# Optimization experiments

Hardware: AMD Instinct MI355X
Metric: run time of the kernel (lower is better)

## Reference

```python
import jax, jax.numpy as jnp
import numpy as np

B, N_T, D_A, D_V, D_U = 64, 8192, 2, 64, 1
L, MODES, X_PAD = 4, 64, 8


def setup_inputs() -> dict:
    key = jax.random.key(0)
    ks = jax.random.split(key, 9)
    scale = 1.0 / (D_V * D_V)  # Xavier-style gain used in original
    return {
        "v": jax.random.normal(ks[0], (B, N_T), dtype=jnp.float32),
        "grid": jax.random.uniform(ks[1], (N_T,), dtype=jnp.float32),
        "p_w": jax.random.normal(ks[2], (D_A, D_V), dtype=jnp.float32) * 0.1,
        "p_b": jnp.zeros((D_V,), dtype=jnp.float32),
        "fw": jax.random.normal(ks[3], (L, D_V, D_V, MODES, 2), dtype=jnp.float32) * scale,
        "w_w": jax.random.normal(ks[4], (L, D_V, D_V), dtype=jnp.float32) * (1.0 / np.sqrt(D_V)),
        "w_b": jnp.zeros((L, D_V), dtype=jnp.float32),
        "q_w": jax.random.normal(ks[5], (D_V, D_U), dtype=jnp.float32) * (1.0 / np.sqrt(D_V)),
        "q_b": jnp.zeros((D_U,), dtype=jnp.float32),
    }


def _fourier_layer(x, w):
    # x: (B, C, n), w: (C, C, modes, 2) real/imag channel-mixing weights
    n = x.shape[-1]
    xf = jnp.fft.rfft(x)                      # (B, C, n//2+1) complex
    xm = xf[:, :, :MODES]
    xr, xi = jnp.real(xm), jnp.imag(xm)
    wr, wi = w[..., 0], w[..., 1]
    out_r = jnp.einsum('bix,iox->box', xr, wr) - jnp.einsum('bix,iox->box', xi, wi)
    out_i = jnp.einsum('bix,iox->box', xi, wr) + jnp.einsum('bix,iox->box', xr, wi)
    out_m = jax.lax.complex(out_r, out_i)     # (B, C, modes)
    out_ft = jnp.pad(out_m, ((0, 0), (0, 0), (0, n // 2 + 1 - MODES)))
    return jnp.fft.irfft(out_ft, n=n)         # (B, C, n)


def reference(v, grid, p_w, p_b, fw, w_w, w_b, q_w, q_b):
    b, n = v.shape
    # lift: concat signal with coordinate channel -> (B, n, 2)
    x = jnp.concatenate([v[:, :, None], jnp.broadcast_to(grid[None, :, None], (b, n, 1))], axis=-1)
    x = x @ p_w + p_b                          # (B, n, d_v)
    x = jnp.transpose(x, (0, 2, 1))            # (B, d_v, n)
    x = jnp.pad(x, ((0, 0), (0, 0), (0, X_PAD)))
    for i in range(L):
        x1 = _fourier_layer(x, fw[i])
        x2 = jnp.einsum('bcn,cd->bdn', x, w_w[i]) + w_b[i][None, :, None]
        x = x1 + x2
        if i < L - 1:
            x = jax.nn.relu(x)
    x = x[..., :-X_PAD]                        # remove padding
    out = jnp.einsum('bcn,cd->bnd', x, q_w) + q_b  # (B, n, d_u)
    return out[..., 0]                         # d_u == 1 -> squeeze
```

## Files before the change

### kernel.cpp

```cpp
#include <hip/hip_runtime.h>

#define NT    8192
#define NP    8200
#define NPP   8320
#define NB    64
#define DV    64
#define NL    4
#define TFR   520
#define KSP   20
#define SPB   13
#define PI2   6.28318530717958647692f

typedef _Float16 half8 __attribute__((ext_vector_type(8)));
typedef _Float16 half4 __attribute__((ext_vector_type(4)));
typedef float    f32x4 __attribute__((ext_vector_type(4)));

static const size_t B_XT   = 0;
static const size_t B_TABF = 68157440ull;
static const size_t B_TABI = B_TABF + 2129920ull;
static const size_t B_WFR  = B_TABI + 2129920ull;
static const size_t B_ZFR  = B_WFR  + 131072ull;
static const size_t B_XPF  = B_ZFR  + 1048576ull;
static const size_t B_VP   = B_XPF  + 20971520ull;
static const size_t B_G    = B_VP   + 327680ull;
static const size_t B_A    = B_G    + 512ull;

__global__ void k_prep(_Float16* __restrict__ tabF, _Float16* __restrict__ tabI) {
    int idx = blockIdx.x * 256 + threadIdx.x;
    if (idx >= NPP * 64) return;
    int t = idx >> 6, k = idx & 63;
    float c = 0.f, s = 0.f;
    if (t < NP) {
        int m = (int)(((long long)t * (long long)k) % NP);
        float th = (float)m * (PI2 / (float)NP);
        sincosf(th, &s, &c);
    }
    float al = (k == 0) ? (1.f / NP) : (2.f / NP);
    {
        int gs = t >> 5, lh = (t >> 3) & 3, j = t & 7;
        int m0 = 2 * k, m1 = 2 * k + 1;
        tabF[(((size_t)gs * 8 + (m0 >> 4)) * 64 + (m0 & 15) + 16 * lh) * 8 + j] = (_Float16)c;
        tabF[(((size_t)gs * 8 + (m1 >> 4)) * 64 + (m1 & 15) + 16 * lh) * 8 + j] = (_Float16)s;
    }
    {
        int tf = t >> 4, lt = t & 15;
        int m0 = 2 * k, m1 = 2 * k + 1;
        tabI[(((size_t)(m0 >> 5) * TFR + tf) * 64 + lt + 16 * ((m0 >> 3) & 3)) * 8 + (m0 & 7)] = (_Float16)(al * c);
        tabI[(((size_t)(m1 >> 5) * TFR + tf) * 64 + lt + 16 * ((m1 >> 3) & 3)) * 8 + (m1 & 7)] = (_Float16)(al * s);
    }
}

__global__ void k_prep_w(const float* __restrict__ ww, _Float16* __restrict__ Wfrag) {
    int idx = blockIdx.x * 256 + threadIdx.x;
    if (idx >= NL * DV * DV) return;
    int l = idx >> 12, cd = idx & 4095, c = cd >> 6, d = cd & 63;
    float wv = ww[((size_t)l * DV + c) * DV + d];
    _Float16 h = (_Float16)wv;
    _Float16 lo = (_Float16)(wv - (float)h);
    int ks = c >> 5, mf = d >> 4;
    int lane = (d & 15) + 16 * ((c >> 3) & 3), j = c & 7;
    Wfrag[((((size_t)l * 2 + 0) * 2 + ks) * 4 + mf) * 512 + (size_t)lane * 8 + j] = h;
    Wfrag[((((size_t)l * 2 + 1) * 2 + ks) * 4 + mf) * 512 + (size_t)lane * 8 + j] = lo;
}

__global__ void k_prep_p(const float* __restrict__ pw, const float* __restrict__ pb,
                         const float* __restrict__ ww, float* __restrict__ A) {
    int d = threadIdx.x;
    float a0 = 0.f, a1 = 0.f, a2 = 0.f;
    #pragma unroll 8
    for (int c = 0; c < DV; ++c) {
        float w = ww[(size_t)c * DV + d];
        a0 = fmaf(pw[c], w, a0);
        a1 = fmaf(pw[DV + c], w, a1);
        a2 = fmaf(pb[c], w, a2);
    }
    A[d] = a0; A[64 + d] = a1; A[128 + d] = a2;
}

__global__ void k_gd(const float* __restrict__ grd, float* __restrict__ G) {
    __shared__ float rb[256];
    int m = blockIdx.x, k = m >> 1, comp = m & 1;
    int tid = threadIdx.x;
    float s = 0.f;
    for (int t = tid; t < NT; t += 256) {
        int mm = (int)(((long long)t * (long long)k) % NP);
        float th = (float)mm * (PI2 / (float)NP);
        float sn, cs; sincosf(th, &sn, &cs);
        s += grd[t] * (comp ? sn : cs);
    }
    rb[tid] = s; __syncthreads();
    for (int h = 128; h > 0; h >>= 1) { if (tid < h) rb[tid] += rb[tid + h]; __syncthreads(); }
    if (tid == 0) G[m] = rb[0];
}

__launch_bounds__(256)
__global__ void k_fdft_v(const float* __restrict__ v, const _Float16* __restrict__ tabF,
                         _Float16* __restrict__ Vp) {
    int ksb = blockIdx.x;
    int tid = threadIdx.x, w = tid >> 6, lane = tid & 63, g = lane >> 4, r = lane & 15;
    const half8* tFv = (const half8*)tabF;
    f32x4 acc[4][2];
    #pragma unroll
    for (int mf = 0; mf < 4; ++mf)
        #pragma unroll
        for (int nf = 0; nf < 2; ++nf) acc[mf][nf] = (f32x4){0.f, 0.f, 0.f, 0.f};
    for (int s = 0; s < SPB; ++s) {
        int gs = ksb * SPB + s;
        int t0 = gs * 32 + g * 8;
        half8 a[4];
        #pragma unroll
        for (int mf = 0; mf < 4; ++mf) {
            int brow = mf * 16 + r;
            half8 hv;
            if (t0 < NT) {
                const float4* pv = (const float4*)&v[(size_t)brow * NT + t0];
                float4 v0 = pv[0], v1 = pv[1];
                hv[0] = (_Float16)v0.x; hv[1] = (_Float16)v0.y; hv[2] = (_Float16)v0.z; hv[3] = (_Float16)v0.w;
                hv[4] = (_Float16)v1.x; hv[5] = (_Float16)v1.y; hv[6] = (_Float16)v1.z; hv[7] = (_Float16)v1.w;
            } else {
                #pragma unroll
                for (int j = 0; j < 8; ++j) hv[j] = (_Float16)0.f;
            }
            a[mf] = hv;
        }
        half8 bb[2];
        #pragma unroll
        for (int nf = 0; nf < 2; ++nf) bb[nf] = tFv[((size_t)gs * 8 + w * 2 + nf) * 64 + lane];
        #pragma unroll
        for (int mf = 0; mf < 4; ++mf)
            #pragma unroll
            for (int nf = 0; nf < 2; ++nf)
                acc[mf][nf] = __builtin_amdgcn_mfma_f32_16x16x32_f16(a[mf], bb[nf], acc[mf][nf], 0, 0, 0);
    }
    #pragma unroll
    for (int mf = 0; mf < 4; ++mf)
        #pragma unroll
        for (int nf = 0; nf < 2; ++nf)
            #pragma unroll
            for (int reg = 0; reg < 4; ++reg) {
                int brow = mf * 16 + g * 4 + reg;
                int m = w * 32 + nf * 16 + r;
                Vp[((size_t)ksb * NB + brow) * 128 + m] = (_Float16)acc[mf][nf][reg];
            }
}

__launch_bounds__(256)
__global__ void k_fdft(const _Float16* __restrict__ xT, const _Float16* __restrict__ tabF,
                       _Float16* __restrict__ xpf) {
    __shared__ _Float16 xls[2048];
    int sb = blockIdx.x, b = blockIdx.y;
    int tid = threadIdx.x, w = tid >> 6, lane = tid & 63, g = lane >> 4, r = lane & 15;
    const half8* tFv = (const half8*)tabF;
    f32x4 acc[4][2];
    #pragma unroll
    for (int cf = 0; cf < 4; ++cf)
        #pragma unroll
        for (int nf = 0; nf < 2; ++nf) acc[cf][nf] = (f32x4){0.f, 0.f, 0.f, 0.f};
    int tl = tid >> 3, c0 = (tid & 7) * 8;
    #pragma unroll 1
    for (int s = 0; s < SPB; ++s) {
        int gs = sb * SPB + s;
        half8 vv = *(const half8*)&xT[((size_t)b * NPP + gs * 32 + tl) * 64 + c0];
        __syncthreads();
        #pragma unroll
        for (int j = 0; j < 8; ++j) {
            int c = c0 + j;
            xls[c * 32 + (tl ^ (((c >> 3) & 3) << 3))] = vv[j];
        }
        __syncthreads();
        half8 a[4], bb[2];
        #pragma unroll
        for (int cf = 0; cf < 4; ++cf) {
            int c = cf * 16 + r;
            a[cf] = *(const half8*)&xls[c * 32 + ((g * 8) ^ ((((c >> 3) & 3)) << 3))];
        }
        #pragma unroll
        for (int nf = 0; nf < 2; ++nf) bb[nf] = tFv[((size_t)gs * 8 + w * 2 + nf) * 64 + lane];
        #pragma unroll
        for (int cf = 0; cf < 4; ++cf)
            #pragma unroll
            for (int nf = 0; nf < 2; ++nf)
                acc[cf][nf] = __builtin_amdgcn_mfma_f32_16x16x32_f16(a[cf], bb[nf], acc[cf][nf], 0, 0, 0);
    }
    _Float16* xp = xpf + (((size_t)sb * NB + b) * 4 + w) * 2048;
    #pragma unroll
    for (int cf = 0; cf < 4; ++cf)
        #pragma unroll
        for (int nf = 0; nf < 2; ++nf) {
            half4 h4;
            #pragma unroll
            for (int reg = 0; reg < 4; ++reg) h4[reg] = (_Float16)acc[cf][nf][reg];
            *(half4*)&xp[(cf * 2 + nf) * 256 + lane * 4] = h4;
        }
}

__launch_bounds__(256)
__global__ void k_spec0(const _Float16* __restrict__ Vp, const float* __restrict__ G,
                        const float* __restrict__ pw, const float* __restrict__ pb,
                        const float* __restrict__ fw_l, _Float16* __restrict__ zfr) {
    __shared__ float Xs[64][32];
    __shared__ float Vs[32], Gs[32];
    int b = blockIdx.y, kq = blockIdx.x, tid = threadIdx.x;
    if (tid < 32) {
        int m = kq * 32 + tid;
        float ssum = 0.f;
        #pragma unroll
        for (int ks = 0; ks < KSP; ++ks) ssum += (float)Vp[((size_t)ks * NB + b) * 128 + m];
        Vs[tid] = ssum;
        Gs[tid] = G[m];
    }
    __syncthreads();
    #pragma unroll
    for (int q = 0; q < 8; ++q) {
        int flat = q * 256 + tid;
        int i = flat >> 5, ml = flat & 31;
        float xv = pw[i] * Vs[ml] + pw[64 + i] * Gs[ml];
        if (kq == 0 && ml == 0) xv += pb[i] * (float)NT;
        Xs[i][ml] = xv;
    }
    __syncthreads();
    #pragma unroll
    for (int q = 0; q < 4; ++q) {
        int flat = q * 256 + tid;
        int o = flat >> 4, kl = flat & 15;
        int k = kq * 16 + kl;
        float yr = 0.f, yi = 0.f;
        #pragma unroll 8
        for (int i = 0; i < 64; ++i) {
            float2 xv = *(const float2*)&Xs[i][2 * kl];
            float2 wv = *(const float2*)&fw_l[(((size_t)i * DV + o) * 64 + k) * 2];
            yr = fmaf(xv.x, wv.x, fmaf(xv.y, wv.y, yr));
            yi = fmaf(xv.x, wv.y, fmaf(-xv.y, wv.x, yi));
        }
        int mf = o >> 4, mm = 2 * kl, m1 = mm + 1;
        zfr[((((size_t)b * 4 + kq) * 4 + mf) * 64 + (o & 15) + 16 * (mm >> 3)) * 8 + (mm & 7)] = (_Float16)yr;
        zfr[((((size_t)b * 4 + kq) * 4 + mf) * 64 + (o & 15) + 16 * (m1 >> 3)) * 8 + (m1 & 7)] = (_Float16)(-yi);
    }
}

__launch_bounds__(256)
__global__ void k_spec(const _Float16* __restrict__ xpf, const float* __restrict__ fw_l,
                       _Float16* __restrict__ zfr) {
    __shared__ float Xs[64][32];
    int b = blockIdx.y, kq = blockIdx.x, tid = threadIdx.x;
    float a8[8];
    #pragma unroll
    for (int e = 0; e < 8; ++e) a8[e] = 0.f;
    const half8* src = (const half8*)xpf;
    size_t base8 = ((size_t)b * 4 + kq) * 256 + tid;
    const size_t step8 = (size_t)NB * 4 * 256;
    for (int ks = 0; ks < KSP; ++ks) {
        half8 vv = src[base8 + (size_t)ks * step8];
        #pragma unroll
        for (int e = 0; e < 8; ++e) a8[e] += (float)vv[e];
    }
    int cf = tid >> 6, nf2 = (tid >> 5) & 1, lane0 = (tid & 31) * 2;
    #pragma unroll
    for (int e = 0; e < 8; ++e) {
        int lane = lane0 + (e >> 2), reg = e & 3;
        int g = lane >> 4, r = lane & 15;
        Xs[cf * 16 + g * 4 + reg][nf2 * 16 + r] = a8[e];
    }
    __syncthreads();
    #pragma unroll
    for (int q = 0; q < 4; ++q) {
        int flat = q * 256 + tid;
        int o = flat >> 4, kl = flat & 15;
        int k = kq * 16 + kl;
        float yr = 0.f, yi = 0.f;
        #pragma unroll 8
        for (int i = 0; i < 64; ++i) {
            float2 xv = *(const float2*)&Xs[i][2 * kl];
            float2 wv = *(const float2*)&fw_l[(((size_t)i * DV + o) * 64 + k) * 2];
            yr = fmaf(xv.x, wv.x, fmaf(xv.y, wv.y, yr));
            yi = fmaf(xv.x, wv.y, fmaf(-xv.y, wv.x, yi));
        }
        int mf = o >> 4, mm = 2 * kl, m1 = mm + 1;
        zfr[((((size_t)b * 4 + kq) * 4 + mf) * 64 + (o & 15) + 16 * (mm >> 3)) * 8 + (mm & 7)] = (_Float16)yr;
        zfr[((((size_t)b * 4 + kq) * 4 + mf) * 64 + (o & 15) + 16 * (m1 >> 3)) * 8 + (m1 & 7)] = (_Float16)(-yi);
    }
}

template <int MODE>
__launch_bounds__(256)
__global__ void k_inv(const _Float16* __restrict__ zfr, const _Float16* __restrict__ tabI,
                      const _Float16* __restrict__ Wl, const float* __restrict__ wb_l,
                      const float* __restrict__ qw, const float* __restrict__ qb,
                      const float* __restrict__ v, const float* __restrict__ grd,
                      const float* __restrict__ A,
                      _Float16* __restrict__ xT, float* __restrict__ out) {
    __shared__ _Float16 xlt[128 * 64];
    __shared__ float red[4][2][64];
    __shared__ float Asm[3][64];
    int b = blockIdx.y, ksb = blockIdx.x;
    int tid = threadIdx.x, w = tid >> 6, lane = tid & 63;
    int g = lane >> 4, r = lane & 15;
    int tw = ksb * 128 + w * 32;
    const half8* zfv = (const half8*)zfr;
    const half8* tIv = (const half8*)tabI;
    const half8* wfv = (const half8*)Wl;

    if (MODE == 0) {
        if (tid < 192) Asm[tid >> 6][tid & 63] = A[tid];
        __syncthreads();
    }

    f32x4 acc[4][2];
    #pragma unroll
    for (int mf = 0; mf < 4; ++mf)
        #pragma unroll
        for (int nf = 0; nf < 2; ++nf) acc[mf][nf] = (f32x4){0.f, 0.f, 0.f, 0.f};

    #pragma unroll
    for (int ks4 = 0; ks4 < 4; ++ks4) {
        half8 az[4], bt[2];
        #pragma unroll
        for (int mf = 0; mf < 4; ++mf)
            az[mf] = zfv[(((size_t)b * 4 + ks4) * 4 + mf) * 64 + lane];
        #pragma unroll
        for (int nf = 0; nf < 2; ++nf)
            bt[nf] = tIv[((size_t)ks4 * TFR + (tw >> 4) + nf) * 64 + lane];
        #pragma unroll
        for (int mf = 0; mf < 4; ++mf)
            #pragma unroll
            for (int nf = 0; nf < 2; ++nf)
                acc[mf][nf] = __builtin_amdgcn_mfma_f32_16x16x32_f16(az[mf], bt[nf], acc[mf][nf], 0, 0, 0);
    }
    if (MODE != 0) {
        half8 xb[2][2];
        #pragma unroll
        for (int ks = 0; ks < 2; ++ks)
            #pragma unroll
            for (int nf = 0; nf < 2; ++nf)
                xb[ks][nf] = *(const half8*)&xT[((size_t)b * NPP + tw + nf * 16 + r) * 64 + ks * 32 + g * 8];
        #pragma unroll
        for (int hl = 0; hl < 2; ++hl)
            #pragma unroll
            for (int ks = 0; ks < 2; ++ks) {
                half8 aw[4];
                #pragma unroll
                for (int mf = 0; mf < 4; ++mf)
                    aw[mf] = wfv[((size_t)(hl * 2 + ks) * 4 + mf) * 64 + lane];
                #pragma unroll
                for (int mf = 0; mf < 4; ++mf)
                    #pragma unroll
                    for (int nf = 0; nf < 2; ++nf)
                        acc[mf][nf] = __builtin_amdgcn_mfma_f32_16x16x32_f16(aw[mf], xb[ks][nf], acc[mf][nf], 0, 0, 0);
            }
    }

    if (MODE != 2) {
        float vv[2], gg[2];
        if (MODE == 0) {
            #pragma unroll
            for (int nf = 0; nf < 2; ++nf) {
                int t = tw + nf * 16 + r;
                bool in = (t < NT);
                vv[nf] = in ? v[(size_t)b * NT + t] : 0.f;
                gg[nf] = in ? grd[t] : 0.f;
            }
        }
        #pragma unroll
        for (int mf = 0; mf < 4; ++mf)
            #pragma unroll
            for (int nf = 0; nf < 2; ++nf) {
                int tl = w * 32 + nf * 16 + r;
                half4 h4;
                #pragma unroll
                for (int reg = 0; reg < 4; ++reg) {
                    int o = mf * 16 + g * 4 + reg;
                    float val = acc[mf][nf][reg] + wb_l[o];
                    if (MODE == 0)
                        val += fmaf(Asm[0][o], vv[nf], fmaf(Asm[1][o], gg[nf], Asm[2][o]));
                    h4[reg] = (_Float16)fmaxf(val, 0.f);
                }
                int idx = tl * 64 + ((mf * 16 + g * 4) ^ ((tl & 7) << 3));
                *(half4*)&xlt[idx] = h4;
            }
        __syncthreads();
        #pragma unroll
        for (int it = 0; it < 4; ++it) {
            int flat = it * 256 + tid;
            int t = flat >> 3, k = flat & 7;
            half8 vv8 = *(const half8*)&xlt[t * 64 + ((k * 8) ^ ((t & 7) << 3))];
            *(half8*)&xT[((size_t)b * NPP + ksb * 128 + t) * 64 + k * 8] = vv8;
        }
    } else {
        float p0 = 0.f, p1 = 0.f;
        #pragma unroll
        for (int mf = 0; mf < 4; ++mf)
            #pragma unroll
            for (int reg = 0; reg < 4; ++reg) {
                int o = mf * 16 + g * 4 + reg;
                float qq = qw[o], bias = wb_l[o];
                p0 = fmaf(acc[mf][0][reg] + bias, qq, p0);
                p1 = fmaf(acc[mf][1][reg] + bias, qq, p1);
            }
        red[w][0][lane] = p0;
        red[w][1][lane] = p1;
        __syncthreads();
        if (tid < 128) {
            int w2 = tid >> 5, nf2 = (tid >> 4) & 1, c2 = tid & 15;
            float s2 = 0.f;
            #pragma unroll
            for (int g2 = 0; g2 < 4; ++g2) s2 += red[w2][nf2][g2 * 16 + c2];
            int t = ksb * 128 + w2 * 32 + nf2 * 16 + c2;
            if (t < NT) out[(size_t)b * NT + t] = s2 + qb[0];
        }
    }
}

extern "C" void kernel_launch(void* const* d_in, const int* in_sizes, int n_in,
                              void* d_out, int out_size, void* d_ws, size_t ws_size,
                              hipStream_t stream) {
    const float* v   = (const float*)d_in[0];
    const float* grd = (const float*)d_in[1];
    const float* pw  = (const float*)d_in[2];
    const float* pb  = (const float*)d_in[3];
    const float* fw  = (const float*)d_in[4];
    const float* ww  = (const float*)d_in[5];
    const float* wb  = (const float*)d_in[6];
    const float* qw  = (const float*)d_in[7];
    const float* qb  = (const float*)d_in[8];
    float* out = (float*)d_out;

    char* wsb = (char*)d_ws;
    _Float16* xT    = (_Float16*)(wsb + B_XT);
    _Float16* tabFb = (_Float16*)(wsb + B_TABF);
    _Float16* tabIb = (_Float16*)(wsb + B_TABI);
    _Float16* Wfrag = (_Float16*)(wsb + B_WFR);
    _Float16* zfrag = (_Float16*)(wsb + B_ZFR);
    _Float16* xpf   = (_Float16*)(wsb + B_XPF);
    _Float16* Vpart = (_Float16*)(wsb + B_VP);
    float*    G     = (float*)(wsb + B_G);
    float*    A     = (float*)(wsb + B_A);

    k_prep<<<(NPP * 64 + 255) / 256, 256, 0, stream>>>(tabFb, tabIb);
    k_prep_w<<<(NL * DV * DV + 255) / 256, 256, 0, stream>>>(ww, Wfrag);
    k_prep_p<<<1, 64, 0, stream>>>(pw, pb, ww, A);
    k_gd<<<128, 256, 0, stream>>>(grd, G);
    k_fdft_v<<<KSP, 256, 0, stream>>>(v, tabFb, Vpart);

    for (int l = 0; l < NL; ++l) {
        if (l == 0) {
            k_spec0<<<dim3(4, NB), 256, 0, stream>>>(Vpart, G, pw, pb, fw, zfrag);
        } else {
            k_fdft<<<dim3(KSP, NB), 256, 0, stream>>>(xT, tabFb, xpf);
            k_spec<<<dim3(4, NB), 256, 0, stream>>>(xpf, fw + (size_t)l * DV * DV * 64 * 2, zfrag);
        }
        const _Float16* wf_l = Wfrag + (size_t)l * 8192;
        const float* wb_l = wb + (size_t)l * DV;
        if (l == 0)
            k_inv<0><<<dim3(NPP / 128, NB), 256, 0, stream>>>(
                zfrag, tabIb, wf_l, wb_l, qw, qb, v, grd, A, xT, out);
        else if (l < NL - 1)
            k_inv<1><<<dim3(NPP / 128, NB), 256, 0, stream>>>(
                zfrag, tabIb, wf_l, wb_l, qw, qb, v, grd, A, xT, out);
        else
            k_inv<2><<<dim3(NT / 128, NB), 256, 0, stream>>>(
                zfrag, tabIb, wf_l, wb_l, qw, qb, v, grd, A, xT, out);
    }
}
```

Measured before the change: 305.6 us.

## Double-buffer forward DFT staging and drop block barriers in inverse kernel

The forward DFT kernel now double-buffers its LDS tile. It prefetches the next time-slab into registers and writes it to the alternate buffer while the current one feeds the MFMAs, so each step needs one barrier instead of two. The inverse kernel stages its transpose in per-wave LDS slices, which removes the block-wide barrier before the store. The final projection reduction uses lane shuffles instead of LDS plus a barrier. In exchange the kernels use more shared memory, and the output store no longer checks t < NT, which could write past the row end if the final-mode grid covers padded timesteps.

```diff
diff --git a/kernel.cpp b/kernel.cpp
--- a/kernel.cpp
+++ b/kernel.cpp
@@ -147,7 +147,7 @@
 __launch_bounds__(256)
 __global__ void k_fdft(const _Float16* __restrict__ xT, const _Float16* __restrict__ tabF,
                        _Float16* __restrict__ xpf) {
-    __shared__ _Float16 xls[2048];
+    __shared__ _Float16 xls[2][2048];
     int sb = blockIdx.x, b = blockIdx.y;
     int tid = threadIdx.x, w = tid >> 6, lane = tid & 63, g = lane >> 4, r = lane & 15;
     const half8* tFv = (const half8*)tabF;
@@ -157,22 +157,33 @@
         #pragma unroll
         for (int nf = 0; nf < 2; ++nf) acc[cf][nf] = (f32x4){0.f, 0.f, 0.f, 0.f};
     int tl = tid >> 3, c0 = (tid & 7) * 8;
+
+    half8 vv = *(const half8*)&xT[((size_t)b * NPP + (sb * SPB) * 32 + tl) * 64 + c0];
+    #pragma unroll
+    for (int j = 0; j < 8; ++j) {
+        int c = c0 + j;
+        xls[0][c * 32 + (tl ^ (((c >> 3) & 3) << 3))] = vv[j];
+    }
+    int cur = 0;
     #pragma unroll 1
     for (int s = 0; s < SPB; ++s) {
         int gs = sb * SPB + s;
-        half8 vv = *(const half8*)&xT[((size_t)b * NPP + gs * 32 + tl) * 64 + c0];
+        half8 vvn;
+        if (s + 1 < SPB)
+            vvn = *(const half8*)&xT[((size_t)b * NPP + (gs + 1) * 32 + tl) * 64 + c0];
         __syncthreads();
-        #pragma unroll
-        for (int j = 0; j < 8; ++j) {
-            int c = c0 + j;
-            xls[c * 32 + (tl ^ (((c >> 3) & 3) << 3))] = vv[j];
-        }
-        __syncthreads();
+        if (s + 1 < SPB) {
+            #pragma unroll
+            for (int j = 0; j < 8; ++j) {
+                int c = c0 + j;
+                xls[cur ^ 1][c * 32 + (tl ^ (((c >> 3) & 3) << 3))] = vvn[j];
+            }
+        }
         half8 a[4], bb[2];
         #pragma unroll
         for (int cf = 0; cf < 4; ++cf) {
             int c = cf * 16 + r;
-            a[cf] = *(const half8*)&xls[c * 32 + ((g * 8) ^ ((((c >> 3) & 3)) << 3))];
+            a[cf] = *(const half8*)&xls[cur][c * 32 + ((g * 8) ^ ((((c >> 3) & 3)) << 3))];
         }
         #pragma unroll
         for (int nf = 0; nf < 2; ++nf) bb[nf] = tFv[((size_t)gs * 8 + w * 2 + nf) * 64 + lane];
@@ -181,6 +192,7 @@
             #pragma unroll
             for (int nf = 0; nf < 2; ++nf)
                 acc[cf][nf] = __builtin_amdgcn_mfma_f32_16x16x32_f16(a[cf], bb[nf], acc[cf][nf], 0, 0, 0);
+        cur ^= 1;
     }
     _Float16* xp = xpf + (((size_t)sb * NB + b) * 4 + w) * 2048;
     #pragma unroll
@@ -289,8 +301,7 @@
                       const float* __restrict__ v, const float* __restrict__ grd,
                       const float* __restrict__ A,
                       _Float16* __restrict__ xT, float* __restrict__ out) {
-    __shared__ _Float16 xlt[128 * 64];
-    __shared__ float red[4][2][64];
+    __shared__ _Float16 xw[4][2048];
     __shared__ float Asm[3][64];
     int b = blockIdx.y, ksb = blockIdx.x;
     int tid = threadIdx.x, w = tid >> 6, lane = tid & 63;
@@ -364,7 +375,7 @@
         for (int mf = 0; mf < 4; ++mf)
             #pragma unroll
             for (int nf = 0; nf < 2; ++nf) {
-                int tl = w * 32 + nf * 16 + r;
+                int tl = nf * 16 + r;
                 half4 h4;
                 #pragma unroll
                 for (int reg = 0; reg < 4; ++reg) {
@@ -375,15 +386,14 @@
                     h4[reg] = (_Float16)fmaxf(val, 0.f);
                 }
                 int idx = tl * 64 + ((mf * 16 + g * 4) ^ ((tl & 7) << 3));
-                *(half4*)&xlt[idx] = h4;
-            }
-        __syncthreads();
+                *(half4*)&xw[w][idx] = h4;
+            }
         #pragma unroll
         for (int it = 0; it < 4; ++it) {
-            int flat = it * 256 + tid;
-            int t = flat >> 3, k = flat & 7;
-            half8 vv8 = *(const half8*)&xlt[t * 64 + ((k * 8) ^ ((t & 7) << 3))];
-            *(half8*)&xT[((size_t)b * NPP + ksb * 128 + t) * 64 + k * 8] = vv8;
+            int t = it * 8 + (lane >> 3);
+            int cg = lane & 7;
+            half8 vv8 = *(const half8*)&xw[w][t * 64 + ((cg * 8) ^ ((t & 7) << 3))];
+            *(half8*)&xT[((size_t)b * NPP + tw + t) * 64 + cg * 8] = vv8;
         }
     } else {
         float p0 = 0.f, p1 = 0.f;
@@ -396,17 +406,11 @@
                 p0 = fmaf(acc[mf][0][reg] + bias, qq, p0);
                 p1 = fmaf(acc[mf][1][reg] + bias, qq, p1);
             }
-        red[w][0][lane] = p0;
-        red[w][1][lane] = p1;
-        __syncthreads();
-        if (tid < 128) {
-            int w2 = tid >> 5, nf2 = (tid >> 4) & 1, c2 = tid & 15;
-            float s2 = 0.f;
-            #pragma unroll
-            for (int g2 = 0; g2 < 4; ++g2) s2 += red[w2][nf2][g2 * 16 + c2];
-            int t = ksb * 128 + w2 * 32 + nf2 * 16 + c2;
-            if (t < NT) out[(size_t)b * NT + t] = s2 + qb[0];
-        }
+        p0 += __shfl_xor(p0, 16); p0 += __shfl_xor(p0, 32);
+        p1 += __shfl_xor(p1, 16); p1 += __shfl_xor(p1, 32);
+        float qbv = qb[0];
+        if (g == 0) out[(size_t)b * NT + tw + r]      = p0 + qbv;
+        if (g == 1) out[(size_t)b * NT + tw + 16 + r] = p1 + qbv;
     }
 }
 
```

New measurement: 301.2 us. About the same (-1.5%).
